# Kernel optimization log

Measured on AMD Instinct MI355X. Metric: run time of the kernel, lower is better.

Reference implementation:

```python
import jax, jax.numpy as jnp
import numpy as np

B, N, D = 4096, 64, 128
H = 2
M = 3 * D            # model_dim = feat + edge + time
DK = M // H          # d_k = d_v = 192


def setup_inputs() -> dict:
    key = jax.random.key(0)
    ks = jax.random.split(key, 20)
    s = 0.02
    mask = jax.random.randint(ks[6], (B, N), 0, 2).astype(bool)
    mask = mask.at[:, 0].set(False)  # guarantee >=1 valid neighbor per row
    return {
        "src":   jax.random.normal(ks[0], (B, D), jnp.float32),
        "src_t": jax.random.normal(ks[1], (B, 1, D), jnp.float32),
        "src_s": jax.random.normal(ks[2], (B, D), jnp.float32),
        "seq":   jax.random.normal(ks[3], (B, N, D), jnp.float32),
        "seq_t": jax.random.normal(ks[4], (B, N, D), jnp.float32),
        "seq_e": jax.random.normal(ks[5], (B, N, D), jnp.float32),
        "mask":  mask,
        # MapBasedMultiHeadAttention params (torch Linear convention: [out, in])
        "Wq": jax.random.normal(ks[7], (M, M), jnp.float32) * s,
        "Wk": jax.random.normal(ks[8], (M, M), jnp.float32) * s,
        "Wv": jax.random.normal(ks[9], (M, M), jnp.float32) * s,
        "w_map": jax.random.normal(ks[10], (2 * DK,), jnp.float32) * s,
        "Wfc": jax.random.normal(ks[11], (M, M), jnp.float32) * s,
        "bfc": jnp.zeros((M,), jnp.float32),
        "ln_g": jnp.ones((M,), jnp.float32),
        "ln_b": jnp.zeros((M,), jnp.float32),
        # MergeLayer params
        "W1": jax.random.normal(ks[12], (D, M + D), jnp.float32) * s,
        "b1": jnp.zeros((D,), jnp.float32),
        "W2": jax.random.normal(ks[13], (D, D), jnp.float32) * s,
        "b2": jnp.zeros((D,), jnp.float32),
    }


def reference(src, src_t, src_s, seq, seq_t, seq_e, mask,
              Wq, Wk, Wv, w_map, Wfc, bfc, ln_g, ln_b, W1, b1, W2, b2):
    # AttnModel.forward with attn_mode='map', dropout in eval mode.
    q_in = jnp.concatenate([src[:, None, :], src_s[:, None, :], src_t], axis=2)  # [B,1,M]
    k_in = jnp.concatenate([seq, seq_e, seq_t], axis=2)                           # [B,N,M]

    qp = (q_in @ Wq.T).reshape(B, 1, H, DK)   # [B,1,H,dk]
    kp = (k_in @ Wk.T).reshape(B, N, H, DK)   # [B,N,H,dk]
    vp = (k_in @ Wv.T).reshape(B, N, H, DK)   # [B,N,H,dv]

    # weight_map(cat([q,k])) decomposes exactly: w1.q + w2.k (no bias, no nonlinearity before softmax)
    w1, w2 = w_map[:DK], w_map[DK:]
    logit = (jnp.einsum('bqhd,d->bhq', qp, w1)[:, :, :, None]
             + jnp.einsum('bnhd,d->bhn', kp, w2)[:, :, None, :])  # [B,H,1,N]
    logit = jnp.where(mask[:, None, None, :], -1e10, logit)
    attn = jax.nn.softmax(logit, axis=-1)                          # [B,H,1,N]

    out = jnp.einsum('bhqn,bnhd->bqhd', attn, vp).reshape(B, M)    # len_q == 1
    out = jax.nn.leaky_relu(out @ Wfc.T + bfc, negative_slope=0.2)
    out = out + q_in[:, 0, :]                                       # residual
    mu = out.mean(-1, keepdims=True)
    var = ((out - mu) ** 2).mean(-1, keepdims=True)
    out = (out - mu) / jnp.sqrt(var + 1e-5) * ln_g + ln_b           # LayerNorm

    # MergeLayer(output, src)
    x = jnp.concatenate([out, src], axis=1)                         # [B, M+D]
    h = jax.nn.relu(x @ W1.T + b1)
    output = h @ W2.T + b2                                          # [B, D]

    # torch attn after squeeze: [n_head*B, N], head-major
    attn_out = attn[:, :, 0, :].transpose(1, 0, 2).reshape(H * B, N)
    return output, attn_out
```

## Files before the change

### kernel.cpp

```cpp
#include <hip/hip_runtime.h>
#include <hip/hip_bf16.h>

#define B_ 4096
#define N_ 64
#define D_ 128
#define H_ 2
#define M_ 384
#define DK_ 192
#define PADROW 392

#define WS_W1T   1024
#define WS_W2T   66560
#define WS_WVB   82944
#define WS_WFCB  156672
#define WS_CTXB  230400
#define WS_OUTVB 1803264
#define WS_R     2589696
#define WS_TOTAL 4162560

typedef __attribute__((ext_vector_type(8))) short bf16x8;
typedef __attribute__((ext_vector_type(4))) float f32x4;

__device__ __forceinline__ unsigned pk2(float a, float b) {
    __hip_bfloat16 x = __float2bfloat16(a), y = __float2bfloat16(b);
    unsigned short ux = __builtin_bit_cast(unsigned short, x);
    unsigned short uy = __builtin_bit_cast(unsigned short, y);
    return (unsigned)ux | ((unsigned)uy << 16);
}
__device__ __forceinline__ float bflo(int v) { return __builtin_bit_cast(float, (unsigned)v << 16); }
__device__ __forceinline__ float bfhi(int v) { return __builtin_bit_cast(float, (unsigned)v & 0xffff0000u); }
__device__ __forceinline__ unsigned short bf1(float a) {
    return __builtin_bit_cast(unsigned short, __float2bfloat16(a));
}

__global__ __launch_bounds__(256) void prep2(
    const float* __restrict__ Wk, const float* __restrict__ wmap,
    const float* __restrict__ W1, const float* __restrict__ W2,
    const float* __restrict__ Wv, const float* __restrict__ Wfc,
    const void* __restrict__ mask, int* __restrict__ flag,
    unsigned short* __restrict__ wkp, float* __restrict__ W1t, float* __restrict__ W2t,
    unsigned short* __restrict__ Wvb, unsigned short* __restrict__ Wfcb) {
    const int tid = threadIdx.x;
    if (blockIdx.x == 0 && tid == 0) {
        const unsigned int* u = (const unsigned int*)mask;
        bool all01 = true, allf = true;
        for (int i = 0; i < 64; ++i) {
            unsigned int v = u[i];
            if (v != 0u && v != 1u) all01 = false;
            if (v != 0u && v != 0x3f800000u) allf = false;
        }
        *flag = all01 ? 0 : (allf ? 2 : 1);
    }
    const int lane = tid & 63, wave = tid >> 6;
    const int gw = blockIdx.x * 4 + wave;
    if (gw < H_ * M_) {
        const int h = gw / M_, m = gw - h * M_;
        float s = 0.f;
        #pragma unroll
        for (int i = 0; i < 3; ++i) {
            int d = lane + i * 64;
            s += wmap[DK_ + d] * Wk[(size_t)(h * DK_ + d) * M_ + m];
        }
        #pragma unroll
        for (int off = 1; off < 64; off <<= 1) s += __shfl_xor(s, off, 64);
        if (lane == 0) wkp[gw] = bf1(s);
    }
    const int gt = blockIdx.x * 256 + tid;
    const int stride = gridDim.x * 256;
    for (int i = gt + H_ * M_; i < 16 * M_; i += stride) wkp[i] = 0;
    for (int i = gt; i < (M_ + D_) * D_; i += stride) {
        int k = i >> 7, o = i & 127;
        W1t[i] = W1[(size_t)o * (M_ + D_) + k];
    }
    for (int i = gt; i < D_ * D_; i += stride) {
        int k = i >> 7, o = i & 127;
        W2t[i] = W2[(size_t)o * D_ + k];
    }
    for (int i = gt; i < M_ * M_; i += stride) {
        Wvb[i]  = bf1(Wv[i]);
        Wfcb[i] = bf1(Wfc[i]);
    }
}

__global__ __launch_bounds__(512) void attn_v3(
    const float* __restrict__ seq, const float* __restrict__ seqE,
    const float* __restrict__ seqT, const void* __restrict__ mask,
    const unsigned short* __restrict__ wkp, const int* __restrict__ flagp,
    unsigned short* __restrict__ ctxb, float* __restrict__ attn_out) {
    __shared__ __hip_bfloat16 skb[N_ * PADROW];
    __shared__ float slog[H_ * N_];

    const int b = blockIdx.x;
    const int tid = threadIdx.x;
    const int lane = tid & 63;
    const int wave = tid >> 6;
    const int j8 = tid & 15;

    const float* base0 = seq  + (size_t)b * (N_ * D_);
    const float* base1 = seqE + (size_t)b * (N_ * D_);
    const float* base2 = seqT + (size_t)b * (N_ * D_);
    #pragma unroll
    for (int k2 = 0; k2 < 2; ++k2) {
        const int idx8 = k2 * 512 + tid;
        const int n = idx8 >> 4;
        const size_t off = (size_t)idx8 * 8;
        #pragma unroll
        for (int t = 0; t < 3; ++t) {
            const float* bp = (t == 0) ? base0 : (t == 1) ? base1 : base2;
            float4 v0 = *(const float4*)&bp[off];
            float4 v1 = *(const float4*)&bp[off + 4];
            int4 pk;
            pk.x = (int)pk2(v0.x, v0.y); pk.y = (int)pk2(v0.z, v0.w);
            pk.z = (int)pk2(v1.x, v1.y); pk.w = (int)pk2(v1.z, v1.w);
            *(int4*)&skb[n * PADROW + t * 128 + j8 * 8] = pk;
        }
    }
    __syncthreads();

    if (wave < 4) {
        const int lr = lane & 15, lk = (lane >> 4) * 8;
        f32x4 acc = {0.f, 0.f, 0.f, 0.f};
        const __hip_bfloat16* arow = &skb[(wave * 16 + lr) * PADROW + lk];
        const unsigned short* brow = &wkp[lr * M_ + lk];
        #pragma unroll
        for (int s = 0; s < 12; ++s) {
            bf16x8 af = *(const bf16x8*)&arow[s * 32];
            bf16x8 bfr = *(const bf16x8*)&brow[s * 32];
            acc = __builtin_amdgcn_mfma_f32_16x16x32_bf16(af, bfr, acc, 0, 0, 0);
        }
        if (lr < 2) {
            #pragma unroll
            for (int q = 0; q < 4; ++q)
                slog[lr * 64 + wave * 16 + (lane >> 4) * 4 + q] = acc[q];
        }
    }
    __syncthreads();

    if (tid < H_ * N_) {
        const int h = tid >> 6, n = tid & 63;
        float lg = slog[tid];
        const int flag = *flagp;
        int mv;
        if (flag == 0)      mv = ((const int*)mask)[(size_t)b * N_ + n];
        else if (flag == 1) mv = ((const unsigned char*)mask)[(size_t)b * N_ + n];
        else                mv = (((const unsigned int*)mask)[(size_t)b * N_ + n] != 0u) ? 1 : 0;
        if (mv) lg = -INFINITY;
        float mx = lg;
        #pragma unroll
        for (int off = 32; off > 0; off >>= 1) mx = fmaxf(mx, __shfl_xor(mx, off, 64));
        float e = __expf(lg - mx);
        float s = e;
        #pragma unroll
        for (int off = 32; off > 0; off >>= 1) s += __shfl_xor(s, off, 64);
        float a = e / s;
        slog[tid] = a;
        attn_out[((size_t)h * B_ + b) * N_ + n] = a;
    }
    __syncthreads();

    if (tid < 384) {
        const int u = tid >> 2, q = tid & 3;
        const int h = (u >= 48) ? 1 : 0;
        const int m8 = u - h * 48;
        const float* pr = &slog[h * 64];
        float acc[8] = {};
        #pragma unroll
        for (int i = 0; i < 16; ++i) {
            const int n = q * 16 + ((i + q * 4) & 15);
            const float a = pr[n];
            int4 kv = *(const int4*)&skb[n * PADROW + m8 * 8];
            acc[0] += a * bflo(kv.x); acc[1] += a * bfhi(kv.x);
            acc[2] += a * bflo(kv.y); acc[3] += a * bfhi(kv.y);
            acc[4] += a * bflo(kv.z); acc[5] += a * bfhi(kv.z);
            acc[6] += a * bflo(kv.w); acc[7] += a * bfhi(kv.w);
        }
        #pragma unroll
        for (int off = 1; off < 4; off <<= 1)
            #pragma unroll
            for (int j = 0; j < 8; ++j) acc[j] += __shfl_xor(acc[j], off, 64);
        if (q == 0) {
            int4 pk;
            pk.x = (int)pk2(acc[0], acc[1]); pk.y = (int)pk2(acc[2], acc[3]);
            pk.z = (int)pk2(acc[4], acc[5]); pk.w = (int)pk2(acc[6], acc[7]);
            *(int4*)&ctxb[(size_t)b * (H_ * M_) + h * M_ + m8 * 8] = pk;
        }
    }
}

__global__ __launch_bounds__(256) void gemm_v_mfma(
    const unsigned short* __restrict__ ctxb, const unsigned short* __restrict__ Wvb,
    unsigned short* __restrict__ outvb) {
    const int tid = threadIdx.x;
    const int wave = tid >> 6, lane = tid & 63;
    const int i0 = blockIdx.x * 64;
    const int j0 = blockIdx.y * 64;
    const int aOff = (j0 >= DK_) ? M_ : 0;
    const int r0 = i0 + wave * 16;
    const int lr = lane & 15, lk = (lane >> 4) * 8;
    f32x4 acc[4] = {{0,0,0,0},{0,0,0,0},{0,0,0,0},{0,0,0,0}};
    const unsigned short* arow = &ctxb[(size_t)(r0 + lr) * (H_ * M_) + aOff + lk];
    #pragma unroll
    for (int kk = 0; kk < M_; kk += 32) {
        bf16x8 af = *(const bf16x8*)&arow[kk];
        #pragma unroll
        for (int jn = 0; jn < 4; ++jn) {
            bf16x8 bfr = *(const bf16x8*)&Wvb[(size_t)(j0 + jn * 16 + lr) * M_ + kk + lk];
            acc[jn] = __builtin_amdgcn_mfma_f32_16x16x32_bf16(af, bfr, acc[jn], 0, 0, 0);
        }
    }
    #pragma unroll
    for (int jn = 0; jn < 4; ++jn)
        #pragma unroll
        for (int q = 0; q < 4; ++q) {
            int row = r0 + (lane >> 4) * 4 + q;
            outvb[(size_t)row * M_ + j0 + jn * 16 + lr] = bf1(acc[jn][q]);
        }
}

__global__ __launch_bounds__(256) void gemm_fc_mfma(
    const unsigned short* __restrict__ outvb, const unsigned short* __restrict__ Wfcb,
    const float* __restrict__ bfc,
    const float* __restrict__ src, const float* __restrict__ src_s, const float* __restrict__ src_t,
    float* __restrict__ rws) {
    const int tid = threadIdx.x;
    const int wave = tid >> 6, lane = tid & 63;
    const int i0 = blockIdx.x * 64;
    const int j0 = blockIdx.y * 64;
    const int r0 = i0 + wave * 16;
    const int lr = lane & 15, lk = (lane >> 4) * 8;
    f32x4 acc[4] = {{0,0,0,0},{0,0,0,0},{0,0,0,0},{0,0,0,0}};
    const unsigned short* arow = &outvb[(size_t)(r0 + lr) * M_ + lk];
    #pragma unroll
    for (int kk = 0; kk < M_; kk += 32) {
        bf16x8 af = *(const bf16x8*)&arow[kk];
        #pragma unroll
        for (int jn = 0; jn < 4; ++jn) {
            bf16x8 bfr = *(const bf16x8*)&Wfcb[(size_t)(j0 + jn * 16 + lr) * M_ + kk + lk];
            acc[jn] = __builtin_amdgcn_mfma_f32_16x16x32_bf16(af, bfr, acc[jn], 0, 0, 0);
        }
    }
    const float* qsrc = (j0 < D_) ? src : (j0 < 2 * D_) ? src_s : src_t;
    const int joff = j0 % D_;
    #pragma unroll
    for (int jn = 0; jn < 4; ++jn)
        #pragma unroll
        for (int q = 0; q < 4; ++q) {
            int row = r0 + (lane >> 4) * 4 + q;
            int jc = jn * 16 + lr;
            float t = acc[jn][q] + bfc[j0 + jc];
            t = t > 0.f ? t : 0.2f * t;
            t += qsrc[(size_t)row * D_ + joff + jc];
            rws[(size_t)row * M_ + j0 + jc] = t;
        }
}

__global__ __launch_bounds__(256) void ln_mlp(
    const float* __restrict__ rin, const float* __restrict__ src,
    const float* __restrict__ g, const float* __restrict__ bta,
    const float* __restrict__ W1t, const float* __restrict__ b1,
    const float* __restrict__ W2t, const float* __restrict__ b2,
    float* __restrict__ outp) {
    __shared__ float sa[8 * 520];
    __shared__ float sh[8 * 132];
    const int b0 = blockIdx.x * 8;
    const int tid = threadIdx.x;
    const int row = tid >> 5, part = tid & 31;
    const size_t gr = (size_t)(b0 + row);
    {
        const float* rr = &rin[gr * M_];
        float4 v[3];
        float s = 0.f, sq = 0.f;
        #pragma unroll
        for (int i = 0; i < 3; ++i) {
            v[i] = *(const float4*)&rr[(part + i * 32) * 4];
            s  += v[i].x + v[i].y + v[i].z + v[i].w;
            sq += v[i].x * v[i].x + v[i].y * v[i].y + v[i].z * v[i].z + v[i].w * v[i].w;
        }
        #pragma unroll
        for (int off = 1; off < 32; off <<= 1) {
            s += __shfl_xor(s, off, 64); sq += __shfl_xor(sq, off, 64);
        }
        float mu = s * (1.f / 384.f);
        float rs = rsqrtf(sq * (1.f / 384.f) - mu * mu + 1e-5f);
        #pragma unroll
        for (int i = 0; i < 3; ++i) {
            int k = (part + i * 32) * 4;
            float4 g4 = *(const float4*)&g[k];
            float4 b4 = *(const float4*)&bta[k];
            float4 z;
            z.x = (v[i].x - mu) * rs * g4.x + b4.x;
            z.y = (v[i].y - mu) * rs * g4.y + b4.y;
            z.z = (v[i].z - mu) * rs * g4.z + b4.z;
            z.w = (v[i].w - mu) * rs * g4.w + b4.w;
            *(float4*)&sa[row * 520 + k] = z;
        }
        *(float4*)&sa[row * 520 + M_ + part * 4] = *(const float4*)&src[gr * D_ + part * 4];
    }
    __syncthreads();
    const int c4 = part * 4;
    float acc[4] = {};
    const float* ar = &sa[row * 520];
    #pragma unroll 4
    for (int k4 = 0; k4 < 128; ++k4) {
        float4 a4 = *(const float4*)&ar[k4 * 4];
        #pragma unroll
        for (int j = 0; j < 4; ++j) {
            int k = k4 * 4 + j;
            float a = (j == 0) ? a4.x : (j == 1) ? a4.y : (j == 2) ? a4.z : a4.w;
            float4 w = *(const float4*)&W1t[k * D_ + c4];
            acc[0] += a * w.x; acc[1] += a * w.y; acc[2] += a * w.z; acc[3] += a * w.w;
        }
    }
    {
        float4 bb = *(const float4*)&b1[c4];
        float4 hh;
        hh.x = fmaxf(acc[0] + bb.x, 0.f);
        hh.y = fmaxf(acc[1] + bb.y, 0.f);
        hh.z = fmaxf(acc[2] + bb.z, 0.f);
        hh.w = fmaxf(acc[3] + bb.w, 0.f);
        *(float4*)&sh[row * 132 + c4] = hh;
    }
    __syncthreads();
    float acc2[4] = {};
    const float* hr = &sh[row * 132];
    #pragma unroll 4
    for (int k4 = 0; k4 < 32; ++k4) {
        float4 a4 = *(const float4*)&hr[k4 * 4];
        #pragma unroll
        for (int j = 0; j < 4; ++j) {
            int k = k4 * 4 + j;
            float a = (j == 0) ? a4.x : (j == 1) ? a4.y : (j == 2) ? a4.z : a4.w;
            float4 w = *(const float4*)&W2t[k * D_ + c4];
            acc2[0] += a * w.x; acc2[1] += a * w.y; acc2[2] += a * w.z; acc2[3] += a * w.w;
        }
    }
    float4 bb2 = *(const float4*)&b2[c4];
    float4 oo = make_float4(acc2[0] + bb2.x, acc2[1] + bb2.y, acc2[2] + bb2.z, acc2[3] + bb2.w);
    *(float4*)&outp[gr * D_ + c4] = oo;
}

extern "C" void kernel_launch(void* const* d_in, const int* in_sizes, int n_in,
                              void* d_out, int out_size, void* d_ws, size_t ws_size,
                              hipStream_t stream) {
    (void)in_sizes; (void)n_in; (void)out_size;
    const float* src   = (const float*)d_in[0];
    const float* src_t = (const float*)d_in[1];
    const float* src_s = (const float*)d_in[2];
    const float* seq   = (const float*)d_in[3];
    const float* seq_t = (const float*)d_in[4];
    const float* seq_e = (const float*)d_in[5];
    const void*  mask  = d_in[6];
    const float* Wk    = (const float*)d_in[8];
    const float* Wv    = (const float*)d_in[9];
    const float* wmap  = (const float*)d_in[10];
    const float* Wfc   = (const float*)d_in[11];
    const float* bfc   = (const float*)d_in[12];
    const float* ln_g  = (const float*)d_in[13];
    const float* ln_b  = (const float*)d_in[14];
    const float* W1    = (const float*)d_in[15];
    const float* b1    = (const float*)d_in[16];
    const float* W2    = (const float*)d_in[17];
    const float* b2    = (const float*)d_in[18];

    if (ws_size < (size_t)WS_TOTAL * sizeof(float)) return;
    float* wsf   = (float*)d_ws;
    int*   flagp = (int*)d_ws;
    float* W1t   = wsf + WS_W1T;
    float* W2t   = wsf + WS_W2T;
    unsigned short* Wvb   = (unsigned short*)(wsf + WS_WVB);
    unsigned short* Wfcb  = (unsigned short*)(wsf + WS_WFCB);
    unsigned short* ctxb  = (unsigned short*)(wsf + WS_CTXB);
    unsigned short* outvb = (unsigned short*)(wsf + WS_OUTVB);
    float* rws   = wsf + WS_R;
    unsigned short* wkp = (unsigned short*)rws;
    float* outp     = (float*)d_out;
    float* attn_out = outp + (size_t)B_ * D_;

    prep2<<<256, 256, 0, stream>>>(Wk, wmap, W1, W2, Wv, Wfc, mask, flagp,
                                   wkp, W1t, W2t, Wvb, Wfcb);
    attn_v3<<<B_, 512, 0, stream>>>(seq, seq_e, seq_t, mask, wkp, flagp, ctxb, attn_out);
    gemm_v_mfma<<<dim3(64, 6), 256, 0, stream>>>(ctxb, Wvb, outvb);
    gemm_fc_mfma<<<dim3(64, 6), 256, 0, stream>>>(outvb, Wfcb, bfc, src, src_s, src_t, rws);
    ln_mlp<<<512, 256, 0, stream>>>(rws, src, ln_g, ln_b, W1t, b1, W2t, b2, outp);
}
```

Measured before the change: 172.1 us.

## Fuse logits, softmax and context into one register-streamed pass per batch

Replaces the attention kernel with a single-pass version. Each thread loads its neighbour rows straight from global memory into registers, computes the two head logits in fp32 against a precomputed effective key vector, applies unnormalized exp with masking, and accumulates the exp-weighted context at once. Partial sums from the waves are combined in a small LDS buffer and then normalized, which removes the bf16 LDS staging of the whole key tile, the MFMA logit step and several block barriers. The softmax no longer subtracts the row maximum, so it relies on the logits being small enough that exp cannot overflow. Block size drops from 512 to 256 threads, and register pressure from the 24-wide accumulators may limit occupancy.

```diff
diff --git a/kernel.cpp b/kernel.cpp
--- a/kernel.cpp
+++ b/kernel.cpp
@@ -7,8 +7,8 @@
 #define H_ 2
 #define M_ 384
 #define DK_ 192
-#define PADROW 392
-
+
+#define WS_WKEFF 64
 #define WS_W1T   1024
 #define WS_W2T   66560
 #define WS_WVB   82944
@@ -21,14 +21,6 @@
 typedef __attribute__((ext_vector_type(8))) short bf16x8;
 typedef __attribute__((ext_vector_type(4))) float f32x4;
 
-__device__ __forceinline__ unsigned pk2(float a, float b) {
-    __hip_bfloat16 x = __float2bfloat16(a), y = __float2bfloat16(b);
-    unsigned short ux = __builtin_bit_cast(unsigned short, x);
-    unsigned short uy = __builtin_bit_cast(unsigned short, y);
-    return (unsigned)ux | ((unsigned)uy << 16);
-}
-__device__ __forceinline__ float bflo(int v) { return __builtin_bit_cast(float, (unsigned)v << 16); }
-__device__ __forceinline__ float bfhi(int v) { return __builtin_bit_cast(float, (unsigned)v & 0xffff0000u); }
 __device__ __forceinline__ unsigned short bf1(float a) {
     return __builtin_bit_cast(unsigned short, __float2bfloat16(a));
 }
@@ -38,7 +30,7 @@
     const float* __restrict__ W1, const float* __restrict__ W2,
     const float* __restrict__ Wv, const float* __restrict__ Wfc,
     const void* __restrict__ mask, int* __restrict__ flag,
-    unsigned short* __restrict__ wkp, float* __restrict__ W1t, float* __restrict__ W2t,
+    float* __restrict__ wkeff, float* __restrict__ W1t, float* __restrict__ W2t,
     unsigned short* __restrict__ Wvb, unsigned short* __restrict__ Wfcb) {
     const int tid = threadIdx.x;
     if (blockIdx.x == 0 && tid == 0) {
@@ -63,11 +55,10 @@
         }
         #pragma unroll
         for (int off = 1; off < 64; off <<= 1) s += __shfl_xor(s, off, 64);
-        if (lane == 0) wkp[gw] = bf1(s);
+        if (lane == 0) wkeff[gw] = s;
     }
     const int gt = blockIdx.x * 256 + tid;
     const int stride = gridDim.x * 256;
-    for (int i = gt + H_ * M_; i < 16 * M_; i += stride) wkp[i] = 0;
     for (int i = gt; i < (M_ + D_) * D_; i += stride) {
         int k = i >> 7, o = i & 127;
         W1t[i] = W1[(size_t)o * (M_ + D_) + k];
@@ -82,108 +73,120 @@
     }
 }
 
-__global__ __launch_bounds__(512) void attn_v3(
+__global__ __launch_bounds__(256) void attn_v4(
     const float* __restrict__ seq, const float* __restrict__ seqE,
     const float* __restrict__ seqT, const void* __restrict__ mask,
-    const unsigned short* __restrict__ wkp, const int* __restrict__ flagp,
+    const float* __restrict__ wkeff, const int* __restrict__ flagp,
     unsigned short* __restrict__ ctxb, float* __restrict__ attn_out) {
-    __shared__ __hip_bfloat16 skb[N_ * PADROW];
-    __shared__ float slog[H_ * N_];
+    __shared__ float scacc[4][16][50];
+    __shared__ float swl[2][64];
+    __shared__ float sel[4][2];
 
     const int b = blockIdx.x;
     const int tid = threadIdx.x;
     const int lane = tid & 63;
-    const int wave = tid >> 6;
+    const int wv = tid >> 6;
     const int j8 = tid & 15;
-
-    const float* base0 = seq  + (size_t)b * (N_ * D_);
-    const float* base1 = seqE + (size_t)b * (N_ * D_);
-    const float* base2 = seqT + (size_t)b * (N_ * D_);
-    #pragma unroll
-    for (int k2 = 0; k2 < 2; ++k2) {
-        const int idx8 = k2 * 512 + tid;
-        const int n = idx8 >> 4;
-        const size_t off = (size_t)idx8 * 8;
-        #pragma unroll
-        for (int t = 0; t < 3; ++t) {
-            const float* bp = (t == 0) ? base0 : (t == 1) ? base1 : base2;
-            float4 v0 = *(const float4*)&bp[off];
-            float4 v1 = *(const float4*)&bp[off + 4];
-            int4 pk;
-            pk.x = (int)pk2(v0.x, v0.y); pk.y = (int)pk2(v0.z, v0.w);
-            pk.z = (int)pk2(v1.x, v1.y); pk.w = (int)pk2(v1.z, v1.w);
-            *(int4*)&skb[n * PADROW + t * 128 + j8 * 8] = pk;
-        }
-    }
-    __syncthreads();
-
-    if (wave < 4) {
-        const int lr = lane & 15, lk = (lane >> 4) * 8;
-        f32x4 acc = {0.f, 0.f, 0.f, 0.f};
-        const __hip_bfloat16* arow = &skb[(wave * 16 + lr) * PADROW + lk];
-        const unsigned short* brow = &wkp[lr * M_ + lk];
-        #pragma unroll
-        for (int s = 0; s < 12; ++s) {
-            bf16x8 af = *(const bf16x8*)&arow[s * 32];
-            bf16x8 bfr = *(const bf16x8*)&brow[s * 32];
-            acc = __builtin_amdgcn_mfma_f32_16x16x32_bf16(af, bfr, acc, 0, 0, 0);
-        }
-        if (lr < 2) {
-            #pragma unroll
-            for (int q = 0; q < 4; ++q)
-                slog[lr * 64 + wave * 16 + (lane >> 4) * 4 + q] = acc[q];
-        }
-    }
-    __syncthreads();
-
-    if (tid < H_ * N_) {
-        const int h = tid >> 6, n = tid & 63;
-        float lg = slog[tid];
-        const int flag = *flagp;
+    const int g = tid >> 4;
+    const int flag = *flagp;
+
+    float wr0[24], wr1[24];
+    #pragma unroll
+    for (int t = 0; t < 3; ++t) {
+        float4 a0 = *(const float4*)&wkeff[t * 128 + j8 * 8];
+        float4 a1 = *(const float4*)&wkeff[t * 128 + j8 * 8 + 4];
+        float4 b0 = *(const float4*)&wkeff[M_ + t * 128 + j8 * 8];
+        float4 b1 = *(const float4*)&wkeff[M_ + t * 128 + j8 * 8 + 4];
+        wr0[t*8+0]=a0.x; wr0[t*8+1]=a0.y; wr0[t*8+2]=a0.z; wr0[t*8+3]=a0.w;
+        wr0[t*8+4]=a1.x; wr0[t*8+5]=a1.y; wr0[t*8+6]=a1.z; wr0[t*8+7]=a1.w;
+        wr1[t*8+0]=b0.x; wr1[t*8+1]=b0.y; wr1[t*8+2]=b0.z; wr1[t*8+3]=b0.w;
+        wr1[t*8+4]=b1.x; wr1[t*8+5]=b1.y; wr1[t*8+6]=b1.z; wr1[t*8+7]=b1.w;
+    }
+
+    float cacc0[24], cacc1[24];
+    #pragma unroll
+    for (int j = 0; j < 24; ++j) { cacc0[j] = 0.f; cacc1[j] = 0.f; }
+    float el0 = 0.f, el1 = 0.f;
+
+    const size_t bbase = (size_t)b * (N_ * D_);
+
+    #pragma unroll
+    for (int it = 0; it < 4; ++it) {
+        const int n = g + (it << 4);
+        const size_t off = bbase + (size_t)n * 128 + j8 * 8;
+        float v[24];
+        {
+            float4 va0 = *(const float4*)&seq [off];
+            float4 va1 = *(const float4*)&seq [off + 4];
+            float4 vb0 = *(const float4*)&seqE[off];
+            float4 vb1 = *(const float4*)&seqE[off + 4];
+            float4 vc0 = *(const float4*)&seqT[off];
+            float4 vc1 = *(const float4*)&seqT[off + 4];
+            v[0]=va0.x; v[1]=va0.y; v[2]=va0.z; v[3]=va0.w;
+            v[4]=va1.x; v[5]=va1.y; v[6]=va1.z; v[7]=va1.w;
+            v[8]=vb0.x; v[9]=vb0.y; v[10]=vb0.z; v[11]=vb0.w;
+            v[12]=vb1.x; v[13]=vb1.y; v[14]=vb1.z; v[15]=vb1.w;
+            v[16]=vc0.x; v[17]=vc0.y; v[18]=vc0.z; v[19]=vc0.w;
+            v[20]=vc1.x; v[21]=vc1.y; v[22]=vc1.z; v[23]=vc1.w;
+        }
+        float a0 = 0.f, a1 = 0.f;
+        #pragma unroll
+        for (int j = 0; j < 24; ++j) { a0 += v[j] * wr0[j]; a1 += v[j] * wr1[j]; }
+        #pragma unroll
+        for (int o = 1; o < 16; o <<= 1) {
+            a0 += __shfl_xor(a0, o, 64);
+            a1 += __shfl_xor(a1, o, 64);
+        }
         int mv;
         if (flag == 0)      mv = ((const int*)mask)[(size_t)b * N_ + n];
         else if (flag == 1) mv = ((const unsigned char*)mask)[(size_t)b * N_ + n];
         else                mv = (((const unsigned int*)mask)[(size_t)b * N_ + n] != 0u) ? 1 : 0;
-        if (mv) lg = -INFINITY;
-        float mx = lg;
-        #pragma unroll
-        for (int off = 32; off > 0; off >>= 1) mx = fmaxf(mx, __shfl_xor(mx, off, 64));
-        float e = __expf(lg - mx);
-        float s = e;
-        #pragma unroll
-        for (int off = 32; off > 0; off >>= 1) s += __shfl_xor(s, off, 64);
-        float a = e / s;
-        slog[tid] = a;
-        attn_out[((size_t)h * B_ + b) * N_ + n] = a;
-    }
+        float w0, w1;
+        if (mv) { w0 = 0.f; w1 = 0.f; }
+        else    { w0 = __expf(a0); w1 = __expf(a1); }
+        el0 += w0; el1 += w1;
+        if (j8 == 0) { swl[0][n] = w0; swl[1][n] = w1; }
+        #pragma unroll
+        for (int j = 0; j < 24; ++j) { cacc0[j] += w0 * v[j]; cacc1[j] += w1 * v[j]; }
+    }
+
+    #pragma unroll
+    for (int o = 16; o <= 32; o <<= 1) {
+        #pragma unroll
+        for (int j = 0; j < 24; ++j) {
+            cacc0[j] += __shfl_xor(cacc0[j], o, 64);
+            cacc1[j] += __shfl_xor(cacc1[j], o, 64);
+        }
+    }
+    #pragma unroll
+    for (int o = 1; o < 64; o <<= 1) {
+        el0 += __shfl_xor(el0, o, 64);
+        el1 += __shfl_xor(el1, o, 64);
+    }
+    if (lane < 16) {
+        float* dst = &scacc[wv][lane][0];
+        #pragma unroll
+        for (int j = 0; j < 24; ++j) { dst[j] = cacc0[j]; dst[24 + j] = cacc1[j]; }
+    }
+    if (lane == 0) { sel[wv][0] = el0; sel[wv][1] = el1; }
     __syncthreads();
 
-    if (tid < 384) {
-        const int u = tid >> 2, q = tid & 3;
-        const int h = (u >= 48) ? 1 : 0;
-        const int m8 = u - h * 48;
-        const float* pr = &slog[h * 64];
-        float acc[8] = {};
-        #pragma unroll
-        for (int i = 0; i < 16; ++i) {
-            const int n = q * 16 + ((i + q * 4) & 15);
-            const float a = pr[n];
-            int4 kv = *(const int4*)&skb[n * PADROW + m8 * 8];
-            acc[0] += a * bflo(kv.x); acc[1] += a * bfhi(kv.x);
-            acc[2] += a * bflo(kv.y); acc[3] += a * bfhi(kv.y);
-            acc[4] += a * bflo(kv.z); acc[5] += a * bfhi(kv.z);
-            acc[6] += a * bflo(kv.w); acc[7] += a * bfhi(kv.w);
-        }
-        #pragma unroll
-        for (int off = 1; off < 4; off <<= 1)
-            #pragma unroll
-            for (int j = 0; j < 8; ++j) acc[j] += __shfl_xor(acc[j], off, 64);
-        if (q == 0) {
-            int4 pk;
-            pk.x = (int)pk2(acc[0], acc[1]); pk.y = (int)pk2(acc[2], acc[3]);
-            pk.z = (int)pk2(acc[4], acc[5]); pk.w = (int)pk2(acc[6], acc[7]);
-            *(int4*)&ctxb[(size_t)b * (H_ * M_) + h * M_ + m8 * 8] = pk;
-        }
+    const float l0 = (sel[0][0] + sel[1][0] + sel[2][0] + sel[3][0]) * 0.0625f;
+    const float l1 = (sel[0][1] + sel[1][1] + sel[2][1] + sel[3][1]) * 0.0625f;
+    const float r0i = 1.f / l0, r1i = 1.f / l1;
+
+    for (int o = tid; o < H_ * M_; o += 256) {
+        const int h = (o >= M_) ? 1 : 0;
+        const int m = o - h * M_;
+        const int t = m >> 7, c = m & 127;
+        const int jm = c >> 3, jj = c & 7;
+        const int idx = h * 24 + t * 8 + jj;
+        float s = scacc[0][jm][idx] + scacc[1][jm][idx] + scacc[2][jm][idx] + scacc[3][jm][idx];
+        ctxb[(size_t)b * (H_ * M_) + o] = bf1(s * (h ? r1i : r0i));
+    }
+    if (tid < H_ * N_) {
+        const int h = tid >> 6, n = tid & 63;
+        attn_out[((size_t)h * B_ + b) * N_ + n] = swl[h][n] * (h ? r1i : r0i);
     }
 }
 
@@ -365,6 +368,7 @@
     if (ws_size < (size_t)WS_TOTAL * sizeof(float)) return;
     float* wsf   = (float*)d_ws;
     int*   flagp = (int*)d_ws;
+    float* wkeff = wsf + WS_WKEFF;
     float* W1t   = wsf + WS_W1T;
     float* W2t   = wsf + WS_W2T;
     unsigned short* Wvb   = (unsigned short*)(wsf + WS_WVB);
@@ -372,13 +376,12 @@
     unsigned short* ctxb  = (unsigned short*)(wsf + WS_CTXB);
     unsigned short* outvb = (unsigned short*)(wsf + WS_OUTVB);
     float* rws   = wsf + WS_R;
-    unsigned short* wkp = (unsigned short*)rws;
     float* outp     = (float*)d_out;
     float* attn_out = outp + (size_t)B_ * D_;
 
     prep2<<<256, 256, 0, stream>>>(Wk, wmap, W1, W2, Wv, Wfc, mask, flagp,
-                                   wkp, W1t, W2t, Wvb, Wfcb);
-    attn_v3<<<B_, 512, 0, stream>>>(seq, seq_e, seq_t, mask, wkp, flagp, ctxb, attn_out);
+                                   wkeff, W1t, W2t, Wvb, Wfcb);
+    attn_v4<<<B_, 256, 0, stream>>>(seq, seq_e, seq_t, mask, wkeff, flagp, ctxb, attn_out);
     gemm_v_mfma<<<dim3(64, 6), 256, 0, stream>>>(ctxb, Wvb, outvb);
     gemm_fc_mfma<<<dim3(64, 6), 256, 0, stream>>>(outvb, Wfcb, bfc, src, src_s, src_t, rws);
     ln_mlp<<<512, 256, 0, stream>>>(rws, src, ln_g, ln_b, W1t, b1, W2t, b2, outp);
```

After: 172.5 us. About the same (+0.3%).
